# Kernel optimization log

Hardware: AMD Instinct MI355X
Metric: run time of the kernel (lower is better)

Reference implementation:

```python
import jax, jax.numpy as jnp
import numpy as np

B, N, TOKEN_DIM = 8, 1024, 768
H, D = 12, 64  # n_heads, head_dim


def setup_inputs() -> dict:
    key = jax.random.key(0)
    k1, k2, k3, k4 = jax.random.split(key, 4)
    x = jax.random.normal(k1, (B, N, TOKEN_DIM), dtype=jnp.float32)
    # nn.Linear(token_dim, 3*H*D, bias=False); store as (in, out)
    W_qkv = jax.random.normal(k2, (TOKEN_DIM, 3 * H * D), dtype=jnp.float32) * (TOKEN_DIM ** -0.5)
    # nn.Linear(H*D, token_dim) with bias
    W_out = jax.random.normal(k3, (H * D, TOKEN_DIM), dtype=jnp.float32) * ((H * D) ** -0.5)
    b_out = jax.random.normal(k4, (TOKEN_DIM,), dtype=jnp.float32) * 0.01
    return {"x": x, "W_qkv": W_qkv, "W_out": W_out, "b_out": b_out}


def reference(x, W_qkv, W_out, b_out):
    b, n, _ = x.shape
    qkv = x @ W_qkv                              # (B, N, 3*H*D)
    # Faithful to original: reshape directly to (B, 3, H, N, D)
    qkv = qkv.reshape(b, 3, H, n, D)
    q, k, v = qkv[:, 0], qkv[:, 1], qkv[:, 2]    # each (B, H, N, D)
    scale = D ** -0.5
    scores = jnp.einsum('bhnd,bhmd->bhnm', q, k) * scale
    probs = jax.nn.softmax(scores, axis=-1)
    attn = jnp.einsum('bhnm,bhmd->bhnd', probs, v)  # (B, H, N, D)
    attn = attn.transpose(0, 2, 1, 3).reshape(b, n, H * D)
    out = attn @ W_out + b_out                    # dropout p=0.0 is identity
    return out
```

## Files before the change

### kernel.cpp

```cpp
#include <hip/hip_runtime.h>
#include <math.h>

static constexpr int NB   = 8;
static constexpr int SEQ  = 1024;
static constexpr int TD   = 768;
static constexpr int NH   = 12;
static constexpr int HD   = 64;
static constexpr int QKVC = 3 * NH * HD;

static constexpr size_t BATCH_ELEMS = (size_t)SEQ * QKVC;
static constexpr size_t THIRD_ELEMS = (size_t)NH * SEQ * HD;
static constexpr size_t HEAD_ELEMS  = (size_t)SEQ * HD;

typedef __bf16 bf16x8 __attribute__((ext_vector_type(8)));
typedef __bf16 bf16x4 __attribute__((ext_vector_type(4)));
typedef float  f32x4  __attribute__((ext_vector_type(4)));

#define MFMA16(a, b, c) __builtin_amdgcn_mfma_f32_16x16x32_bf16((a), (b), (c), 0, 0, 0)

static constexpr float SCL2E = 0.18033688011112042f;

__device__ __forceinline__ void gload_lds16(const void* g, void* l) {
  __builtin_amdgcn_global_load_lds(
      (const __attribute__((address_space(1))) unsigned int*)g,
      (__attribute__((address_space(3))) unsigned int*)l, 16, 0, 0);
}

__global__ __launch_bounds__(256) void prep(const float* __restrict__ x,
                                            const float* __restrict__ Wq,
                                            const float* __restrict__ Wo,
                                            __bf16* __restrict__ xb,
                                            __bf16* __restrict__ wqt,
                                            __bf16* __restrict__ wot) {
  const int blk = blockIdx.x;
  const int tid = threadIdx.x;
  if (blk < 6144) {
    int i = blk * 256 + tid;
    float4 v = ((const float4*)x)[i];
    bf16x4 o;
    o[0] = (__bf16)v.x; o[1] = (__bf16)v.y; o[2] = (__bf16)v.z; o[3] = (__bf16)v.w;
    ((bf16x4*)xb)[i] = o;
    return;
  }
  __shared__ float T[32 * 33];
  const float* W;
  __bf16* Wt;
  int K, N, k0, n0;
  if (blk < 6144 + 1728) {
    int bidx = blk - 6144;
    W = Wq; Wt = wqt; K = TD; N = QKVC;
    k0 = (bidx / 72) * 32; n0 = (bidx % 72) * 32;
  } else {
    int bidx = blk - 7872;
    W = Wo; Wt = wot; K = TD; N = TD;
    k0 = (bidx / 24) * 32; n0 = (bidx % 24) * 32;
  }
#pragma unroll
  for (int i = 0; i < 4; ++i) {
    int idx = tid + i * 256;
    int kk = idx >> 5, nn = idx & 31;
    T[kk * 33 + nn] = W[(size_t)(k0 + kk) * N + n0 + nn];
  }
  __syncthreads();
#pragma unroll
  for (int i = 0; i < 4; ++i) {
    int idx = tid + i * 256;
    int nn = idx >> 5, kk = idx & 31;
    Wt[(size_t)(n0 + nn) * K + k0 + kk] = (__bf16)T[kk * 33 + nn];
  }
}

__global__ __launch_bounds__(256) void vtrans(const __bf16* __restrict__ qkvb,
                                              __bf16* __restrict__ vtb) {
  const int nt = blockIdx.x;
  const int h = blockIdx.y;
  const int b = blockIdx.z;
  __shared__ __bf16 T[128 * 72];
  const int tid = threadIdx.x;
  const int n0 = nt * 128;
  const __bf16* Vb = qkvb + (size_t)b * BATCH_ELEMS + 2 * THIRD_ELEMS + (size_t)h * HEAD_ELEMS;
#pragma unroll
  for (int i = 0; i < 4; ++i) {
    int ch = tid + i * 256;
    int row = ch >> 3, c8 = ch & 7;
    *(bf16x8*)&T[row * 72 + c8 * 8] = *(const bf16x8*)&Vb[(size_t)(n0 + row) * HD + c8 * 8];
  }
  __syncthreads();
#pragma unroll
  for (int i = 0; i < 4; ++i) {
    int ch = tid + i * 256;
    int d = ch >> 4, n8 = ch & 15;
    bf16x8 v;
#pragma unroll
    for (int jj = 0; jj < 8; ++jj) {
      int j = (jj + n8) & 7;
      v[j] = T[(n8 * 8 + j) * 72 + d];
    }
    *(bf16x8*)&vtb[((size_t)((b * NH + h) * HD) + d) * SEQ + n0 + n8 * 8] = v;
  }
}

template <int MODE, int BM, int BN>
__global__ __launch_bounds__(256) void gemm_mfma(const __bf16* __restrict__ A,
                                                 const __bf16* __restrict__ Bt,
                                                 const float* __restrict__ bias,
                                                 void* __restrict__ C,
                                                 int M, int N, int K) {
  constexpr int MI = BM / 32;
  constexpr int NJ = BN / 32;
  __shared__ __bf16 As[2][BM * 32];
  __shared__ __bf16 Bs[2][BN * 32];
  const int tid = threadIdx.x;
  const int lane = tid & 63;
  const int wid = tid >> 6;
  const int wr = wid >> 1, wc = wid & 1;
  const int r = lane & 15, g = lane >> 4;
  const size_t bm = (size_t)blockIdx.y * BM;
  const size_t bn = (size_t)blockIdx.x * BN;

  const int srow = lane >> 2;
  const int scol = (lane & 3) * 8;

  auto stage = [&](int buf, int k0) {
#pragma unroll
    for (int j = 0; j < BM / 64; ++j) {
      const int rowbase = wid * (BM / 4) + j * 16;
      gload_lds16(&A[(bm + rowbase + srow) * K + k0 + scol], &As[buf][rowbase * 32]);
    }
#pragma unroll
    for (int j = 0; j < BN / 64; ++j) {
      const int rowbase = wid * (BN / 4) + j * 16;
      gload_lds16(&Bt[(bn + rowbase + srow) * K + k0 + scol], &Bs[buf][rowbase * 32]);
    }
  };

  f32x4 acc[MI][NJ];
#pragma unroll
  for (int mi = 0; mi < MI; ++mi)
#pragma unroll
    for (int nj = 0; nj < NJ; ++nj) acc[mi][nj] = (f32x4){0.f, 0.f, 0.f, 0.f};

  stage(0, 0);
  __syncthreads();

  int cur = 0;
  for (int k0 = 0; k0 < K; k0 += 32) {
    if (k0 + 32 < K) stage(cur ^ 1, k0 + 32);
    bf16x8 af[MI], bf[NJ];
#pragma unroll
    for (int mi = 0; mi < MI; ++mi)
      af[mi] = *(const bf16x8*)&As[cur][(wr * (BM / 2) + mi * 16 + r) * 32 + g * 8];
#pragma unroll
    for (int nj = 0; nj < NJ; ++nj)
      bf[nj] = *(const bf16x8*)&Bs[cur][(wc * (BN / 2) + nj * 16 + r) * 32 + g * 8];
#pragma unroll
    for (int mi = 0; mi < MI; ++mi)
#pragma unroll
      for (int nj = 0; nj < NJ; ++nj)
        acc[mi][nj] = MFMA16(af[mi], bf[nj], acc[mi][nj]);
    __syncthreads();
    cur ^= 1;
  }

  const int orow0 = g * 4;
  const int ocol = r;
#pragma unroll
  for (int mi = 0; mi < MI; ++mi)
#pragma unroll
    for (int nj = 0; nj < NJ; ++nj)
#pragma unroll
      for (int reg = 0; reg < 4; ++reg) {
        size_t rrow = bm + wr * (BM / 2) + mi * 16 + orow0 + reg;
        size_t ccol = bn + wc * (BN / 2) + nj * 16 + ocol;
        float v = acc[mi][nj][reg];
        if (MODE == 1) {
          int fwb = ((int)(rrow & (SEQ - 1))) * QKVC + (int)ccol;
          float vv = (fwb < (int)THIRD_ELEMS) ? v * SCL2E : v;
          ((__bf16*)C)[rrow * N + ccol] = (__bf16)vv;
        } else {
          ((float*)C)[rrow * N + ccol] = v + bias[ccol];
        }
      }
}

__global__ __launch_bounds__(256) void attn_mfma(const __bf16* __restrict__ qkvb,
                                                 const __bf16* __restrict__ vtb,
                                                 __bf16* __restrict__ attn2b) {
  const int d = blockIdx.x;
  const int qt = (d >> 3) & 7;
  const int hb = (d >> 6) * 8 + (d & 7);
  const int b = hb / NH, h = hb % NH;

  const int tid = threadIdx.x;
  const int lane = tid & 63;
  const int w = tid >> 6;
  const int c = lane & 15, g = lane >> 4;

  __shared__ __bf16 KsF[2][4096];
  __shared__ __bf16 VsF[2][4096];

  const __bf16* Qb = qkvb + (size_t)b * BATCH_ELEMS + (size_t)h * HEAD_ELEMS;
  const __bf16* Kb = Qb + THIRD_ELEMS;
  const __bf16* Vtb = vtb + (size_t)((b * NH + h) * HD) * SEQ;

  const f32x4 ZERO4 = {0.f, 0.f, 0.f, 0.f};
  bf16x8 onesf;
#pragma unroll
  for (int i = 0; i < 8; ++i) onesf[i] = (__bf16)1.0f;

  const __bf16* kS[2];
  const __bf16* vS[2];
  int ldsOff[2];
#pragma unroll
  for (int i = 0; i < 2; ++i) {
    const int t2f = i * 4 + w;
    const int t = t2f >> 1, f = t2f & 1;
    const int krow = ((t >> 1) << 5) | ((c >> 2) << 3) | ((t & 1) << 2) | (c & 3);
    kS[i] = Kb + krow * HD + f * 32 + g * 8;
    const int db = t2f >> 1, kk = t2f & 1;
    vS[i] = Vtb + (db * 16 + c) * SEQ + kk * 32 + g * 8;
    ldsOff[i] = t2f * 512;
  }

  bf16x8 qf[2][2];
#pragma unroll
  for (int s = 0; s < 2; ++s) {
    const int q0s = qt * 128 + s * 64 + w * 16;
#pragma unroll
    for (int f = 0; f < 2; ++f)
      qf[s][f] = *(const bf16x8*)&Qb[(size_t)(q0s + c) * HD + f * 32 + g * 8];
  }

  f32x4 Oa[2][4];
  f32x4 La[2];
#pragma unroll
  for (int s = 0; s < 2; ++s) {
#pragma unroll
    for (int db = 0; db < 4; ++db) Oa[s][db] = ZERO4;
    La[s] = ZERO4;
  }

#pragma unroll
  for (int i = 0; i < 2; ++i) {
    gload_lds16(kS[i], &KsF[0][ldsOff[i]]);
    gload_lds16(vS[i], &VsF[0][ldsOff[i]]);
    kS[i] += 64 * HD;
    vS[i] += 64;
  }
  __syncthreads();

  int cur = 0;
  for (int it = 0; it < SEQ / 64; ++it) {
    if (it < SEQ / 64 - 1) {
      const int nxt = cur ^ 1;
#pragma unroll
      for (int i = 0; i < 2; ++i) {
        gload_lds16(kS[i], &KsF[nxt][ldsOff[i]]);
        gload_lds16(vS[i], &VsF[nxt][ldsOff[i]]);
        kS[i] += 64 * HD;
        vS[i] += 64;
      }
    }

    f32x4 sa[2][4];
#pragma unroll
    for (int t = 0; t < 4; ++t) {
      bf16x8 kf0 = *(const bf16x8*)&KsF[cur][(t * 2 + 0) * 512 + lane * 8];
      bf16x8 kf1 = *(const bf16x8*)&KsF[cur][(t * 2 + 1) * 512 + lane * 8];
      sa[0][t] = MFMA16(kf0, qf[0][0], ZERO4);
      sa[1][t] = MFMA16(kf0, qf[1][0], ZERO4);
      sa[0][t] = MFMA16(kf1, qf[0][1], sa[0][t]);
      sa[1][t] = MFMA16(kf1, qf[1][1], sa[1][t]);
    }

    bf16x8 pb[2][2];
#pragma unroll
    for (int s = 0; s < 2; ++s)
#pragma unroll
      for (int kk = 0; kk < 2; ++kk)
#pragma unroll
        for (int i = 0; i < 4; ++i) {
          pb[s][kk][i] = (__bf16)__builtin_exp2f(sa[s][2 * kk][i]);
          pb[s][kk][4 + i] = (__bf16)__builtin_exp2f(sa[s][2 * kk + 1][i]);
        }

#pragma unroll
    for (int kk = 0; kk < 2; ++kk) {
      La[0] = MFMA16(onesf, pb[0][kk], La[0]);
      La[1] = MFMA16(onesf, pb[1][kk], La[1]);
    }
#pragma unroll
    for (int db = 0; db < 4; ++db)
#pragma unroll
      for (int kk = 0; kk < 2; ++kk) {
        bf16x8 vf = *(const bf16x8*)&VsF[cur][(db * 2 + kk) * 512 + lane * 8];
        Oa[0][db] = MFMA16(vf, pb[0][kk], Oa[0][db]);
        Oa[1][db] = MFMA16(vf, pb[1][kk], Oa[1][db]);
      }

    __syncthreads();
    cur ^= 1;
  }

#pragma unroll
  for (int s = 0; s < 2; ++s) {
    const float inv = 1.0f / La[s][0];
    const size_t rowq = (size_t)(b * SEQ) + qt * 128 + s * 64 + w * 16 + c;
#pragma unroll
    for (int db = 0; db < 4; ++db) {
      bf16x4 o;
#pragma unroll
      for (int reg = 0; reg < 4; ++reg) o[reg] = (__bf16)(Oa[s][db][reg] * inv);
      *(bf16x4*)&attn2b[rowq * TD + h * HD + db * 16 + g * 4] = o;
    }
  }
}

extern "C" void kernel_launch(void* const* d_in, const int* in_sizes, int n_in,
                              void* d_out, int out_size, void* d_ws,
                              size_t ws_size, hipStream_t stream) {
  const float* x = (const float*)d_in[0];
  const float* W_qkv = (const float*)d_in[1];
  const float* W_out = (const float*)d_in[2];
  const float* b_out = (const float*)d_in[3];
  float* out = (float*)d_out;

  __bf16* xb = (__bf16*)d_ws;
  __bf16* wqkvt = xb + (size_t)NB * SEQ * TD;
  __bf16* woutt = wqkvt + (size_t)QKVC * TD;
  __bf16* qkvb = woutt + (size_t)TD * TD;
  __bf16* vtb = qkvb + (size_t)NB * SEQ * QKVC;
  __bf16* attn2b = vtb + (size_t)NB * NH * HD * SEQ;

  prep<<<dim3(8448), 256, 0, stream>>>(x, W_qkv, W_out, xb, wqkvt, woutt);

  gemm_mfma<1, 128, 192><<<dim3(QKVC / 192, NB * SEQ / 128), 256, 0, stream>>>(
      xb, wqkvt, nullptr, qkvb, NB * SEQ, QKVC, TD);

  vtrans<<<dim3(SEQ / 128, NH, NB), 256, 0, stream>>>(qkvb, vtb);

  attn_mfma<<<dim3(SEQ / 128 * NH * NB), 256, 0, stream>>>(qkvb, vtb, attn2b);

  gemm_mfma<0, 64, 192><<<dim3(TD / 192, NB * SEQ / 64), 256, 0, stream>>>(
      attn2b, woutt, b_out, out, NB * SEQ, TD, TD);
}
```

Before: 132.4 us.

## Split attention KV sequence into two partitions with a merge kernel

The attention kernel now launches twice as many blocks, each handling half of the key/value sequence (512 keys). Each block writes an unnormalized partial output in bf16 and its row sums to workspace, and a new merge kernel adds the two partials and divides by the combined sum. The aim is more blocks than the 768 previously launched, for better CU occupancy on the 256-CU MI355X. The cost is an extra launch, extra global traffic for the partial outputs, and rounding of the partial outputs to bf16 before normalization. There is no max subtraction, so the split relies on the existing pre-scaled exponentials being summable without a shared max.

```diff
diff --git a/kernel.cpp b/kernel.cpp
--- a/kernel.cpp
+++ b/kernel.cpp
@@ -185,10 +185,14 @@
 
 __global__ __launch_bounds__(256) void attn_mfma(const __bf16* __restrict__ qkvb,
                                                  const __bf16* __restrict__ vtb,
-                                                 __bf16* __restrict__ attn2b) {
-  const int d = blockIdx.x;
-  const int qt = (d >> 3) & 7;
-  const int hb = (d >> 6) * 8 + (d & 7);
+                                                 __bf16* __restrict__ Op0,
+                                                 __bf16* __restrict__ Op1,
+                                                 float* __restrict__ Lp) {
+  const int d0 = blockIdx.x;
+  const int part = d0 >= 768;
+  const int dd = d0 - (part ? 768 : 0);
+  const int qt = (dd >> 3) & 7;
+  const int hb = (dd >> 6) * 8 + (dd & 7);
   const int b = hb / NH, h = hb % NH;
 
   const int tid = threadIdx.x;
@@ -216,9 +220,9 @@
     const int t2f = i * 4 + w;
     const int t = t2f >> 1, f = t2f & 1;
     const int krow = ((t >> 1) << 5) | ((c >> 2) << 3) | ((t & 1) << 2) | (c & 3);
-    kS[i] = Kb + krow * HD + f * 32 + g * 8;
+    kS[i] = Kb + (size_t)(part * 512) * HD + krow * HD + f * 32 + g * 8;
     const int db = t2f >> 1, kk = t2f & 1;
-    vS[i] = Vtb + (db * 16 + c) * SEQ + kk * 32 + g * 8;
+    vS[i] = Vtb + (db * 16 + c) * SEQ + part * 512 + kk * 32 + g * 8;
     ldsOff[i] = t2f * 512;
   }
 
@@ -250,8 +254,8 @@
   __syncthreads();
 
   int cur = 0;
-  for (int it = 0; it < SEQ / 64; ++it) {
-    if (it < SEQ / 64 - 1) {
+  for (int it = 0; it < 8; ++it) {
+    if (it < 7) {
       const int nxt = cur ^ 1;
 #pragma unroll
       for (int i = 0; i < 2; ++i) {
@@ -302,18 +306,40 @@
     cur ^= 1;
   }
 
+  __bf16* Op = part ? Op1 : Op0;
 #pragma unroll
   for (int s = 0; s < 2; ++s) {
-    const float inv = 1.0f / La[s][0];
     const size_t rowq = (size_t)(b * SEQ) + qt * 128 + s * 64 + w * 16 + c;
 #pragma unroll
     for (int db = 0; db < 4; ++db) {
       bf16x4 o;
 #pragma unroll
-      for (int reg = 0; reg < 4; ++reg) o[reg] = (__bf16)(Oa[s][db][reg] * inv);
-      *(bf16x4*)&attn2b[rowq * TD + h * HD + db * 16 + g * 4] = o;
-    }
-  }
+      for (int reg = 0; reg < 4; ++reg) o[reg] = (__bf16)Oa[s][db][reg];
+      *(bf16x4*)&Op[rowq * TD + h * HD + db * 16 + g * 4] = o;
+    }
+    if (g == 0)
+      Lp[((size_t)part * NB * SEQ + rowq) * NH + h] = La[s][0];
+  }
+}
+
+__global__ __launch_bounds__(256) void attn_merge(const __bf16* __restrict__ Op0,
+                                                  const __bf16* __restrict__ Op1,
+                                                  const float* __restrict__ Lp,
+                                                  __bf16* __restrict__ attn2b) {
+  const int idx = blockIdx.x * 256 + threadIdx.x;
+  const int rowq = idx / 192;
+  const int col4 = idx - rowq * 192;
+  const int h = col4 >> 4;
+  const float L = Lp[(size_t)rowq * NH + h] +
+                  Lp[((size_t)NB * SEQ + rowq) * NH + h];
+  const float inv = 1.0f / L;
+  bf16x4 a = ((const bf16x4*)Op0)[idx];
+  bf16x4 b = ((const bf16x4*)Op1)[idx];
+  bf16x4 o;
+#pragma unroll
+  for (int i = 0; i < 4; ++i)
+    o[i] = (__bf16)(((float)a[i] + (float)b[i]) * inv);
+  ((bf16x4*)attn2b)[idx] = o;
 }
 
 extern "C" void kernel_launch(void* const* d_in, const int* in_sizes, int n_in,
@@ -331,6 +357,9 @@
   __bf16* qkvb = woutt + (size_t)TD * TD;
   __bf16* vtb = qkvb + (size_t)NB * SEQ * QKVC;
   __bf16* attn2b = vtb + (size_t)NB * NH * HD * SEQ;
+  __bf16* Opart1 = attn2b + (size_t)NB * SEQ * TD;
+  float* Lpart = (float*)(Opart1 + (size_t)NB * SEQ * TD);
+  __bf16* Opart0 = xb;
 
   prep<<<dim3(8448), 256, 0, stream>>>(x, W_qkv, W_out, xb, wqkvt, woutt);
 
@@ -339,7 +368,10 @@
 
   vtrans<<<dim3(SEQ / 128, NH, NB), 256, 0, stream>>>(qkvb, vtb);
 
-  attn_mfma<<<dim3(SEQ / 128 * NH * NB), 256, 0, stream>>>(qkvb, vtb, attn2b);
+  attn_mfma<<<dim3(2 * SEQ / 128 * NH * NB), 256, 0, stream>>>(
+      qkvb, vtb, Opart0, Opart1, Lpart);
+
+  attn_merge<<<dim3(6144), 256, 0, stream>>>(Opart0, Opart1, Lpart, attn2b);
 
   gemm_mfma<0, 64, 192><<<dim3(TD / 192, NB * SEQ / 64), 256, 0, stream>>>(
       attn2b, woutt, b_out, out, NB * SEQ, TD, TD);
```

New measurement: 142.3 us. 7.5% more time.
